# Optimization experiments

Hardware: AMD Instinct MI355X
Metric: run time of the kernel (lower is better)

Reference implementation:

```python
import jax, jax.numpy as jnp
import numpy as np
from jax import lax

_T, _B, _I, _H = 2048, 1024, 15, 10


def setup_inputs() -> dict:
    key = jax.random.key(0)
    k1, k2, k3, k4, k5 = jax.random.split(key, 5)
    s = 1.0 / np.sqrt(_H)  # PyTorch LSTM init range
    return {
        "x": jax.random.normal(k1, (_T, _B, _I), dtype=jnp.float32),
        "h0": jax.random.normal(k2, (1, _B, _H), dtype=jnp.float32),
        "c0": jax.random.normal(k3, (1, _B, _H), dtype=jnp.float32),
        "W_ih": jax.random.uniform(k4, (4 * _H, _I), dtype=jnp.float32, minval=-s, maxval=s),
        "W_hh": jax.random.uniform(k5, (4 * _H, _H), dtype=jnp.float32, minval=-s, maxval=s),
    }


def _lstm(x, h0, c0, W_ih, W_hh):
    # Precompute input contribution for all timesteps: (T, B, 4H)
    pre = jnp.einsum('tbi,gi->tbg', x, W_ih)

    def step(carry, pre_t):
        h, c = carry  # (B, H) each
        gates = pre_t + h @ W_hh.T  # (B, 4H)
        i, f, g, o = jnp.split(gates, 4, axis=-1)  # PyTorch gate order i,f,g,o
        i = jax.nn.sigmoid(i)
        f = jax.nn.sigmoid(f)
        g = jnp.tanh(g)
        o = jax.nn.sigmoid(o)
        c = f * c + i * g
        h = o * jnp.tanh(c)
        return (h, c), h

    (hT, cT), out = lax.scan(step, (h0[0], c0[0]), pre)
    return out, hT[None, :, :], cT[None, :, :]


def reference(x, h0, c0, W_ih, W_hh):
    out, hN, cN = _lstm(x, h0, c0, W_ih, W_hh)
    return out, hN, cN
```

## Files before the change

### kernel.cpp

```cpp
#include <hip/hip_runtime.h>


#define T_N  2048
#define B_N  1024
#define I_N  15
#define H_N  10
#define DQ   32
#define NBLK (T_N / DQ)
#define LPAD 64

typedef _Float16 f16x8  __attribute__((ext_vector_type(8)));
typedef float    f32x16 __attribute__((ext_vector_type(16)));

template <int CTRL>
static __device__ __forceinline__ float dppf(float v) {
    return __builtin_bit_cast(float,
        __builtin_amdgcn_mov_dpp(__builtin_bit_cast(int, v), CTRL, 0xF, 0xF, true));
}
static __device__ __forceinline__ float rl(float v, int lane) {
    return __builtin_bit_cast(float, __builtin_amdgcn_readlane(__builtin_bit_cast(int, v), lane));
}

#define BAR() asm volatile("s_waitcnt lgkmcnt(0)\n\ts_barrier" ::: "memory")

#define CSTEP(xav) do {                                                           \
    float d0 = fmaf(hs0, wh0, (xav)); d0 = fmaf(hs5, wh5, d0);                    \
    float d1 = hs1 * wh1;             d1 = fmaf(hs6, wh6, d1);                    \
    float d2 = hs2 * wh2;             d2 = fmaf(hs7, wh7, d2);                    \
    float d3 = hs3 * wh3;             d3 = fmaf(hs8, wh8, d3);                    \
    float d4 = hs4 * wh4;             d4 = fmaf(hs9, wh9, d4);                    \
    const float acc = (d0 + d1 + d2) + (d3 + d4);                                 \
    const float e   = __builtin_amdgcn_exp2f(acc);                                \
    const float rc  = __builtin_amdgcn_rcpf(1.0f + e);                            \
    const float act = fmaf(Aact, rc, Bact);                                       \
    const float iv  = dppf<0x00>(act);                                            \
    const float fv  = dppf<0x55>(act);                                            \
    const float gv  = dppf<0xAA>(act);                  \
    const float ov  = dppf<0xFF>(act);                                            \
    const float ovm2 = -2.0f * ov;                                 \
    cs = fmaf(fv, cs, iv * gv);                              \
    const float tt = __builtin_amdgcn_exp2f(cs);                                  \
    const float rr = __builtin_amdgcn_rcpf(1.0f + tt);                            \
    h = fmaf(ovm2, rr, ov);                                                       \
    hs0 = rl(h, 0);  hs1 = rl(h, 4);  hs2 = rl(h, 8);  hs3 = rl(h, 12);           \
    hs4 = rl(h, 16); hs5 = rl(h, 20); hs6 = rl(h, 24); hs7 = rl(h, 28);           \
    hs8 = rl(h, 32); hs9 = rl(h, 36);                                             \
} while (0)

#define CBLOCK(PAR) do {                                                          \
    float xa[DQ];                                                                 \
    _Pragma("unroll")                                                             \
    for (int d = 0; d < DQ; ++d) xa[d] = buf[PAR][d][crow];                       \
    _Pragma("unroll")                                                             \
    for (int d = 0; d < DQ; ++d) { CSTEP(xa[d]); hsh[PAR][d][lane] = h; }         \
} while (0)

#define PLOADX(KB) do {                                                           \
    int t = (KB) * DQ + trow; if (t > T_N - 1) t = T_N - 1;                       \
    const float* xp = x + ((size_t)t * B_N + b) * I_N + koff;                     \
    _Pragma("unroll")                                                             \
    for (int e = 0; e < 8; ++e) xr[e] = (koff + e < I_N) ? xp[e] : 0.0f;          \
} while (0)

#define PPROJ(PAR) do {                                                           \
    f16x8 af;                                                                     \
    _Pragma("unroll")                                                             \
    for (int e = 0; e < 8; ++e) af[e] = (_Float16)xr[e];                          \
    const f32x16 dA = __builtin_amdgcn_mfma_f32_32x32x16_f16(af, bf0, z16, 0, 0, 0); \
    const f32x16 dB = __builtin_amdgcn_mfma_f32_32x32x16_f16(af, bf1, z16, 0, 0, 0); \
    _Pragma("unroll")                                                             \
    for (int r = 0; r < 16; ++r) {                                                \
        const int rw = (r & 3) + 8 * (r >> 2) + rbase;                            \
        buf[PAR][rw][ncol]      = dA[r];                                          \
        buf[PAR][rw][ncol + 32] = dB[r];                                          \
    }                                                                             \
} while (0)

#define HSTORE(MB) do {                                                           \
    const int par_ = (MB) & 1;                                                    \
    if (sact) {                                                                   \
        _Pragma("unroll")                                                         \
        for (int r = 0; r < 6; ++r) {                                             \
            const int dd = r * 6 + sl_d;                                          \
            if (dd < DQ)                                                          \
                out[((size_t)(MB) * DQ + dd) * (B_N * H_N) + b * H_N + sl_j]      \
                    = hsh[par_][dd][4 * sl_j];                                    \
        }                                                                         \
    }                                                                             \
} while (0)

__global__ __launch_bounds__(128, 2)
void lstm_pc(const float* __restrict__ x, const float* __restrict__ h0,
             const float* __restrict__ c0, const float* __restrict__ Wih,
             const float* __restrict__ Whh, float* __restrict__ out)
{
    __shared__ float buf[2][DQ][LPAD];
    __shared__ float hsh[2][DQ][64];

    const int tid  = threadIdx.x;
    const int wave = tid >> 6;
    const int lane = tid & 63;
    const int b    = blockIdx.x;
    const float LOG2E = 1.4426950408889634f;

    const int trow  = lane & 31;
    const int koff  = (lane >> 5) * 8;
    const int ncol  = lane & 31;
    const int rbase = 4 * (lane >> 5);
    const int sl_j  = lane % H_N;
    const int sl_d  = lane / H_N;
    const bool sact = lane < 60;
    f16x8 bf0, bf1;
    f32x16 z16;
    float xr[8];

    const int p = lane & 3;
    int j = lane >> 2; if (j > H_N - 1) j = H_N - 1;
    const int crow = p * H_N + j;
    const bool writer = (wave == 0) && (p == 0) && (lane < 4 * H_N);
    const float Aact = (p == 2) ? -4.0f * LOG2E : 1.0f;
    const float Bact = (p == 2) ?  2.0f * LOG2E : 0.0f;
    float wh0, wh1, wh2, wh3, wh4, wh5, wh6, wh7, wh8, wh9;
    float cs, h;
    float hs0, hs1, hs2, hs3, hs4, hs5, hs6, hs7, hs8, hs9;

    if (wave == 1) {
        __builtin_amdgcn_s_setprio(0);
#pragma unroll
        for (int e = 0; e < 8; ++e) {
            const int k = koff + e;
            {
                const int n = ncol;
                const float sgn = (n >= 20 && n < 30) ? 2.0f * LOG2E : -LOG2E;
                bf0[e] = (_Float16)((k < I_N) ? sgn * Wih[n * I_N + k] : 0.0f);
            }
            {
                const int n = 32 + ncol;
                const float sgn = (n >= 20 && n < 30) ? 2.0f * LOG2E : -LOG2E;
                bf1[e] = (_Float16)((k < I_N && n < 40) ? sgn * Wih[n * I_N + k] : 0.0f);
            }
        }
#pragma unroll
        for (int r = 0; r < 16; ++r) z16[r] = 0.0f;
        PLOADX(0);
        PPROJ(0);
        PLOADX(1);
    } else {
        __builtin_amdgcn_s_setprio(1);
        const float sg = (p == 2) ? 2.0f * LOG2E : -LOG2E;
        const float* wr = Whh + crow * H_N;
        wh0 = sg * wr[0]; wh1 = sg * wr[1]; wh2 = sg * wr[2]; wh3 = sg * wr[3];
        wh4 = sg * wr[4]; wh5 = sg * wr[5]; wh6 = sg * wr[6]; wh7 = sg * wr[7];
        wh8 = sg * wr[8]; wh9 = sg * wr[9];
        cs = c0[b * H_N + j] * (2.0f * LOG2E);
        h  = h0[b * H_N + j];
        hs0 = rl(h, 0);  hs1 = rl(h, 4);  hs2 = rl(h, 8);  hs3 = rl(h, 12);
        hs4 = rl(h, 16); hs5 = rl(h, 20); hs6 = rl(h, 24); hs7 = rl(h, 28);
        hs8 = rl(h, 32); hs9 = rl(h, 36);
    }
    BAR();

    for (int m = 0; m < NBLK; ++m) {
        if (wave == 1) {
            PPROJ((m + 1) & 1);
            PLOADX(m + 2);
            if (m > 0) HSTORE(m - 1);
        } else {
            CBLOCK(m & 1);
        }
        BAR();
    }

    if (wave == 1) {
        HSTORE(NBLK - 1);
    } else if (writer) {
        const size_t base = (size_t)T_N * B_N * H_N;
        out[base + b * H_N + j] = h;
        out[base + (size_t)B_N * H_N + b * H_N + j] = cs * 0.34657359027997264f;
    }
}

extern "C" void kernel_launch(void* const* d_in, const int* in_sizes, int n_in,
                              void* d_out, int out_size, void* d_ws, size_t ws_size,
                              hipStream_t stream) {
    const float* x   = (const float*)d_in[0];
    const float* h0  = (const float*)d_in[1];
    const float* c0  = (const float*)d_in[2];
    const float* Wih = (const float*)d_in[3];
    const float* Whh = (const float*)d_in[4];
    float* out = (float*)d_out;
    lstm_pc<<<dim3(B_N), dim3(128), 0, stream>>>(x, h0, c0, Wih, Whh, out);
}
```

Before: 190.4 us.

## Use packed fp16 dot2 for recurrent matvec and triple-buffer pre-activations

```diff
diff --git a/kernel.cpp b/kernel.cpp
--- a/kernel.cpp
+++ b/kernel.cpp
@@ -9,8 +9,9 @@
 #define NBLK (T_N / DQ)
 #define LPAD 64
 
-typedef _Float16 f16x8  __attribute__((ext_vector_type(8)));
-typedef float    f32x16 __attribute__((ext_vector_type(16)));
+typedef _Float16 half2_t __attribute__((ext_vector_type(2)));
+typedef _Float16 f16x8   __attribute__((ext_vector_type(8)));
+typedef float    f32x16  __attribute__((ext_vector_type(16)));
 
 template <int CTRL>
 static __device__ __forceinline__ float dppf(float v) {
@@ -20,16 +21,22 @@
 static __device__ __forceinline__ float rl(float v, int lane) {
     return __builtin_bit_cast(float, __builtin_amdgcn_readlane(__builtin_bit_cast(int, v), lane));
 }
+static __device__ __forceinline__ unsigned rlu(unsigned v, int lane) {
+    return (unsigned)__builtin_amdgcn_readlane((int)v, lane);
+}
+static __device__ __forceinline__ half2_t h2(unsigned u) {
+    return __builtin_bit_cast(half2_t, u);
+}
 
 #define BAR() asm volatile("s_waitcnt lgkmcnt(0)\n\ts_barrier" ::: "memory")
 
 #define CSTEP(xav) do {                                                           \
-    float d0 = fmaf(hs0, wh0, (xav)); d0 = fmaf(hs5, wh5, d0);                    \
-    float d1 = hs1 * wh1;             d1 = fmaf(hs6, wh6, d1);                    \
-    float d2 = hs2 * wh2;             d2 = fmaf(hs7, wh7, d2);                    \
-    float d3 = hs3 * wh3;             d3 = fmaf(hs8, wh8, d3);                    \
-    float d4 = hs4 * wh4;             d4 = fmaf(hs9, wh9, d4);                    \
-    const float acc = (d0 + d1 + d2) + (d3 + d4);                                 \
+    float A  = __builtin_amdgcn_fdot2(h2(hp0), wf0, (xav), false);                \
+    A        = __builtin_amdgcn_fdot2(h2(hp1), wf1, A,     false);                \
+    float Bv = __builtin_amdgcn_fdot2(h2(hp2), wf2, 0.f,   false);                \
+    Bv       = __builtin_amdgcn_fdot2(h2(hp3), wf3, Bv,    false);                \
+    const float Cv = __builtin_amdgcn_fdot2(h2(hp4), wf4, 0.f, false);            \
+    const float acc = (A + Bv) + Cv;                                              \
     const float e   = __builtin_amdgcn_exp2f(acc);                                \
     const float rc  = __builtin_amdgcn_rcpf(1.0f + e);                            \
     const float act = fmaf(Aact, rc, Bact);                                       \
@@ -42,17 +49,21 @@
     const float tt = __builtin_amdgcn_exp2f(cs);                                  \
     const float rr = __builtin_amdgcn_rcpf(1.0f + tt);                            \
     h = fmaf(ovm2, rr, ov);                                                       \
-    hs0 = rl(h, 0);  hs1 = rl(h, 4);  hs2 = rl(h, 8);  hs3 = rl(h, 12);           \
-    hs4 = rl(h, 16); hs5 = rl(h, 20); hs6 = rl(h, 24); hs7 = rl(h, 28);           \
-    hs8 = rl(h, 32); hs9 = rl(h, 36);                                             \
-} while (0)
-
-#define CBLOCK(PAR) do {                                                          \
-    float xa[DQ];                                                                 \
-    _Pragma("unroll")                                                             \
-    for (int d = 0; d < DQ; ++d) xa[d] = buf[PAR][d][crow];                       \
-    _Pragma("unroll")                                                             \
-    for (int d = 0; d < DQ; ++d) { CSTEP(xa[d]); hsh[PAR][d][lane] = h; }         \
+    const float hbv = dppf<0x104>(h);          \
+    const unsigned pkh = __builtin_bit_cast(unsigned,                             \
+                             __builtin_amdgcn_cvt_pkrtz(h, hbv));                 \
+    hp0 = rlu(pkh, 0); hp1 = rlu(pkh, 8); hp2 = rlu(pkh, 16);                     \
+    hp3 = rlu(pkh, 24); hp4 = rlu(pkh, 32);                                       \
+} while (0)
+
+#define CBLOCK(XC, XN, SLOTN, PAR) do {                                           \
+    const float* nb = &buf[SLOTN][0][crow];                                       \
+    _Pragma("unroll")                                                             \
+    for (int d = 0; d < DQ; ++d) {                                                \
+        CSTEP(XC[d]);                                                             \
+        XN[d] = nb[d * LPAD];                                                     \
+        hsh[PAR][d][lane] = h;                                                    \
+    }                                                                             \
 } while (0)
 
 #define PLOADX(KB) do {                                                           \
@@ -62,7 +73,7 @@
     for (int e = 0; e < 8; ++e) xr[e] = (koff + e < I_N) ? xp[e] : 0.0f;          \
 } while (0)
 
-#define PPROJ(PAR) do {                                                           \
+#define PPROJ(SLOT) do {                                                          \
     f16x8 af;                                                                     \
     _Pragma("unroll")                                                             \
     for (int e = 0; e < 8; ++e) af[e] = (_Float16)xr[e];                          \
@@ -71,8 +82,8 @@
     _Pragma("unroll")                                                             \
     for (int r = 0; r < 16; ++r) {                                                \
         const int rw = (r & 3) + 8 * (r >> 2) + rbase;                            \
-        buf[PAR][rw][ncol]      = dA[r];                                          \
-        buf[PAR][rw][ncol + 32] = dB[r];                                          \
+        buf[SLOT][rw][ncol]      = dA[r];                                         \
+        buf[SLOT][rw][ncol + 32] = dB[r];            \
     }                                                                             \
 } while (0)
 
@@ -94,7 +105,7 @@
              const float* __restrict__ c0, const float* __restrict__ Wih,
              const float* __restrict__ Whh, float* __restrict__ out)
 {
-    __shared__ float buf[2][DQ][LPAD];
+    __shared__ float buf[3][DQ][LPAD];
     __shared__ float hsh[2][DQ][64];
 
     const int tid  = threadIdx.x;
@@ -120,9 +131,10 @@
     const bool writer = (wave == 0) && (p == 0) && (lane < 4 * H_N);
     const float Aact = (p == 2) ? -4.0f * LOG2E : 1.0f;
     const float Bact = (p == 2) ?  2.0f * LOG2E : 0.0f;
-    float wh0, wh1, wh2, wh3, wh4, wh5, wh6, wh7, wh8, wh9;
+    half2_t wf0, wf1, wf2, wf3, wf4;
     float cs, h;
-    float hs0, hs1, hs2, hs3, hs4, hs5, hs6, hs7, hs8, hs9;
+    unsigned hp0, hp1, hp2, hp3, hp4;
+    float xqA[DQ], xqB[DQ];
 
     if (wave == 1) {
         __builtin_amdgcn_s_setprio(0);
@@ -145,30 +157,53 @@
         PLOADX(0);
         PPROJ(0);
         PLOADX(1);
+        PPROJ(1);
+        PLOADX(2);
     } else {
         __builtin_amdgcn_s_setprio(1);
         const float sg = (p == 2) ? 2.0f * LOG2E : -LOG2E;
         const float* wr = Whh + crow * H_N;
-        wh0 = sg * wr[0]; wh1 = sg * wr[1]; wh2 = sg * wr[2]; wh3 = sg * wr[3];
-        wh4 = sg * wr[4]; wh5 = sg * wr[5]; wh6 = sg * wr[6]; wh7 = sg * wr[7];
-        wh8 = sg * wr[8]; wh9 = sg * wr[9];
+        half2_t w;
+        w[0] = (_Float16)(sg * wr[0]); w[1] = (_Float16)(sg * wr[1]); wf0 = w;
+        w[0] = (_Float16)(sg * wr[2]); w[1] = (_Float16)(sg * wr[3]); wf1 = w;
+        w[0] = (_Float16)(sg * wr[4]); w[1] = (_Float16)(sg * wr[5]); wf2 = w;
+        w[0] = (_Float16)(sg * wr[6]); w[1] = (_Float16)(sg * wr[7]); wf3 = w;
+        w[0] = (_Float16)(sg * wr[8]); w[1] = (_Float16)(sg * wr[9]); wf4 = w;
         cs = c0[b * H_N + j] * (2.0f * LOG2E);
         h  = h0[b * H_N + j];
-        hs0 = rl(h, 0);  hs1 = rl(h, 4);  hs2 = rl(h, 8);  hs3 = rl(h, 12);
-        hs4 = rl(h, 16); hs5 = rl(h, 20); hs6 = rl(h, 24); hs7 = rl(h, 28);
-        hs8 = rl(h, 32); hs9 = rl(h, 36);
+        const float hbv = dppf<0x104>(h);
+        const unsigned pkh = __builtin_bit_cast(unsigned,
+                                 __builtin_amdgcn_cvt_pkrtz(h, hbv));
+        hp0 = rlu(pkh, 0); hp1 = rlu(pkh, 8); hp2 = rlu(pkh, 16);
+        hp3 = rlu(pkh, 24); hp4 = rlu(pkh, 32);
     }
     BAR();
 
-    for (int m = 0; m < NBLK; ++m) {
+    if (wave == 0) {
+#pragma unroll
+        for (int d = 0; d < DQ; ++d) xqA[d] = buf[0][d][crow];
+    }
+
+    int slR = 1, slW = 2, slO = 0;
+    for (int m = 0; m < NBLK; m += 2) {
         if (wave == 1) {
-            PPROJ((m + 1) & 1);
-            PLOADX(m + 2);
+            PPROJ(slW);
+            PLOADX(m + 3);
             if (m > 0) HSTORE(m - 1);
         } else {
-            CBLOCK(m & 1);
+            CBLOCK(xqA, xqB, slR, 0);
         }
         BAR();
+        { const int t = slO; slO = slR; slR = slW; slW = t; }
+        if (wave == 1) {
+            PPROJ(slW);
+            PLOADX(m + 4);
+            HSTORE(m);
+        } else {
+            CBLOCK(xqB, xqA, slR, 1);
+        }
+        BAR();
+        { const int t = slO; slO = slR; slR = slW; slW = t; }
     }
 
     if (wave == 1) {
```

Measured after the change: 182.2 us. 1.05x faster.
